# Kernel tuning notes

Measured on AMD Instinct MI355X. Metric: run time of the kernel, lower is better.

## Reference

```python
import jax, jax.numpy as jnp
import numpy as np

T, H, F, E, K = 1024, 2048, 1024, 8, 2  # tokens, hidden, intermediate, experts, top_k
RENORMALIZE = True


def setup_inputs() -> dict:
    key = jax.random.key(0)
    k1, k2, k3, k4, k5 = jax.random.split(key, 5)
    hidden_states = jax.random.normal(k1, (T, H), dtype=jnp.float32)
    router_logits = jax.random.normal(k2, (T, E), dtype=jnp.float32)
    w1 = jax.random.normal(k3, (E, H, F), dtype=jnp.float32) * 0.02  # gate proj
    w3 = jax.random.normal(k4, (E, H, F), dtype=jnp.float32) * 0.02  # up proj
    w2 = jax.random.normal(k5, (E, F, H), dtype=jnp.float32) * 0.02  # down proj
    return {"hidden_states": hidden_states, "router_logits": router_logits,
            "w1": w1, "w3": w3, "w2": w2}


def _moe_forward(x, router_logits, w1, w3, w2):
    # Top-K routing: softmax over all experts, select top-k, optional renormalize.
    probs = jax.nn.softmax(router_logits, axis=-1)            # [T, E]
    topk_vals, topk_ids = jax.lax.top_k(probs, K)             # [T, K]
    if RENORMALIZE:
        topk_vals = topk_vals / jnp.sum(topk_vals, axis=-1, keepdims=True)
    # Dense combine weights: zero for non-selected experts.   [T, E]
    tok_idx = jnp.arange(x.shape[0])[:, None]
    combine = jnp.zeros(probs.shape, dtype=x.dtype).at[tok_idx, topk_ids].set(topk_vals)
    # Expert SwiGLU FFN computed per expert over all tokens, masked-combined.
    g = jnp.einsum('th,ehf->etf', x, w1)                      # gate  [E, T, F]
    u = jnp.einsum('th,ehf->etf', x, w3)                      # up    [E, T, F]
    a = jax.nn.silu(g) * u                                    # silu activation
    y = jnp.einsum('etf,efh->eth', a, w2)                     # down  [E, T, H]
    out = jnp.einsum('eth,te->th', y, combine)                # weighted combine
    return out


def reference(hidden_states, router_logits, w1, w3, w2):
    return _moe_forward(hidden_states, router_logits, w1, w3, w2)
```

## Files before the change

kernel.cpp:

```cpp
#include <hip/hip_runtime.h>
#include <cstdint>
#include <cstddef>

#define T_TOK 1024
#define H_DIM 2048
#define F_DIM 1024
#define E_EXP 8
#define BM 64
#define BK 64
#define BN2 64
#define SP 70
#define MAX_TILES 40
#define ROWCAP 2560

#define I_NTILES 25
#define I_TILE_E 32
#define I_TILE_R0 80
#define I_ROWTOK 4224
#define I_ROWW   6784
#define B_XB     37888
#define B_AWS    (B_XB + T_TOK*H_DIM*2)
#define B_W1T    (B_AWS + ROWCAP*F_DIM*2)
#define B_W3T    (B_W1T + E_EXP*F_DIM*H_DIM*2)

typedef __bf16 bf16x8 __attribute__((ext_vector_type(8)));
typedef __bf16 bf16x2 __attribute__((ext_vector_type(2)));
typedef float  f32x4  __attribute__((ext_vector_type(4)));

#define MFMA(a,b,c) __builtin_amdgcn_mfma_f32_16x16x32_bf16(a,b,c,0,0,0)

__device__ __forceinline__ void gload16(const void* g, void* l) {
  __builtin_amdgcn_global_load_lds(
      (const __attribute__((address_space(1))) void*)g,
      (__attribute__((address_space(3))) void*)l, 16, 0, 0);
}

__global__ __launch_bounds__(1024) void k_route(const float* __restrict__ logits,
                                                int* __restrict__ ws_i) {
  __shared__ int cnt[E_EXP], cur[E_EXP], offs_s[E_EXP];
  const int t = threadIdx.x;
  float* ws_f = (float*)ws_i;
  if (t < E_EXP) { cnt[t] = 0; cur[t] = 0; }
  __syncthreads();
  float l[E_EXP];
#pragma unroll
  for (int e = 0; e < E_EXP; ++e) l[e] = logits[t * E_EXP + e];
  int b0 = 0; float v0 = l[0];
#pragma unroll
  for (int e = 1; e < E_EXP; ++e) if (l[e] > v0) { v0 = l[e]; b0 = e; }
  int b1 = -1; float v1 = -3.4e38f;
#pragma unroll
  for (int e = 0; e < E_EXP; ++e) if (e != b0 && l[e] > v1) { v1 = l[e]; b1 = e; }
  float w0 = 1.f / (1.f + __expf(v1 - v0));
  float w1 = 1.f - w0;
  atomicAdd(&cnt[b0], 1);
  atomicAdd(&cnt[b1], 1);
  __syncthreads();
  if (t == 0) {
    int off = 0, nt = 0;
    for (int e = 0; e < E_EXP; ++e) {
      offs_s[e] = off;
      int ntile = (cnt[e] + BM - 1) / BM;
      for (int i = 0; i < ntile; ++i) {
        ws_i[I_TILE_E + nt] = e;
        ws_i[I_TILE_R0 + nt] = off + i * BM;
        ++nt;
      }
      off += ntile * BM;
    }
    ws_i[I_NTILES] = nt;
  }
  for (int i = t; i < ROWCAP; i += 1024) ws_i[I_ROWTOK + i] = -1;
  __syncthreads();
  {
    int p = atomicAdd(&cur[b0], 1);
    int s = offs_s[b0] + p;
    ws_i[I_ROWTOK + s] = t;
    ws_f[I_ROWW + s] = w0;
  }
  {
    int p = atomicAdd(&cur[b1], 1);
    int s = offs_s[b1] + p;
    ws_i[I_ROWTOK + s] = t;
    ws_f[I_ROWW + s] = w1;
  }
}

__global__ __launch_bounds__(256) void k_cvt(const float* __restrict__ x,
                                             __bf16* __restrict__ xb) {
  long i = (long)(blockIdx.x * 256 + threadIdx.x) * 8;
  float4 a = *(const float4*)(x + i);
  float4 b = *(const float4*)(x + i + 4);
  bf16x8 v;
  v[0] = (__bf16)a.x; v[1] = (__bf16)a.y; v[2] = (__bf16)a.z; v[3] = (__bf16)a.w;
  v[4] = (__bf16)b.x; v[5] = (__bf16)b.y; v[6] = (__bf16)b.z; v[7] = (__bf16)b.w;
  *(bf16x8*)(xb + i) = v;
}

__global__ __launch_bounds__(256) void k_cvtT(const float* __restrict__ src,
                                              __bf16* __restrict__ dst,
                                              int R, int C) {
  __shared__ __bf16 tr[64][66];
  const int e = blockIdx.z, r0 = blockIdx.x * 64, c0 = blockIdx.y * 64;
  const float* s = src + ((size_t)e * R + r0) * C + c0;
  __bf16* d = dst + ((size_t)e * C + c0) * R + r0;
  const int t = threadIdx.x;
  const int lr = t >> 4, lc = (t & 15) * 4;
#pragma unroll
  for (int i = 0; i < 4; ++i) {
    int r = lr + i * 16;
    float4 f = *(const float4*)(s + (size_t)r * C + lc);
    tr[lc + 0][r] = (__bf16)f.x;
    tr[lc + 1][r] = (__bf16)f.y;
    tr[lc + 2][r] = (__bf16)f.z;
    tr[lc + 3][r] = (__bf16)f.w;
  }
  __syncthreads();
  const int oc = t >> 2, ok = (t & 3) * 16;
  *(bf16x8*)(d + (size_t)oc * R + ok)     = *(const bf16x8*)&tr[oc][ok];
  *(bf16x8*)(d + (size_t)oc * R + ok + 8) = *(const bf16x8*)&tr[oc][ok + 8];
}

__global__ __launch_bounds__(256) void k_gemm1(const __bf16* __restrict__ xb,
                                               const __bf16* __restrict__ w1t,
                                               const __bf16* __restrict__ w3t,
                                               const int* __restrict__ ws_i,
                                               __bf16* __restrict__ aws) {
  __shared__ __bf16 sm[2][3 * 4096];
  __shared__ int s_tok[BM];
  const int p = blockIdx.x;
  const int lg = (p & 7) * 80 + (p >> 3);
  const int tile = lg % MAX_TILES;
  const int n0 = (lg / MAX_TILES) * 64;
  if (tile >= ws_i[I_NTILES]) return;
  const int e  = ws_i[I_TILE_E + tile];
  const int r0 = ws_i[I_TILE_R0 + tile];
  const int tid = threadIdx.x, lane = tid & 63, wid = tid >> 6;
  const int wm = wid >> 1, wn = wid & 1;
  const int l15 = lane & 15, l4 = lane >> 4;
  if (tid < BM) {
    int tk = ws_i[I_ROWTOK + r0 + tid];
    s_tok[tid] = tk < 0 ? 0 : tk;
  }
  __syncthreads();
  const int rj0 = wid * 16 + (lane >> 3);
  const int rj1 = rj0 + 8;
  const int ks = ((lane & 7) ^ (lane >> 3)) * 8;
  const __bf16* gA0 = xb + (size_t)s_tok[rj0] * H_DIM + ks;
  const __bf16* gA1 = xb + (size_t)s_tok[rj1] * H_DIM + ks;
  const __bf16* w1e = w1t + (size_t)e * F_DIM * H_DIM;
  const __bf16* w3e = w3t + (size_t)e * F_DIM * H_DIM;
  const __bf16* gB1_0 = w1e + (size_t)(n0 + rj0) * H_DIM + ks;
  const __bf16* gB1_1 = w1e + (size_t)(n0 + rj1) * H_DIM + ks;
  const __bf16* gB3_0 = w3e + (size_t)(n0 + rj0) * H_DIM + ks;
  const __bf16* gB3_1 = w3e + (size_t)(n0 + rj1) * H_DIM + ks;
  const int c0 = wid * 2 * 512, c1 = c0 + 512;

  auto STAGE = [&](int b, int k0) {
    __bf16* As = &sm[b][0];
    __bf16* B1 = &sm[b][4096];
    __bf16* B3 = &sm[b][8192];
    gload16(gA0 + k0,   As + c0);
    gload16(gA1 + k0,   As + c1);
    gload16(gB1_0 + k0, B1 + c0);
    gload16(gB1_1 + k0, B1 + c1);
    gload16(gB3_0 + k0, B3 + c0);
    gload16(gB3_1 + k0, B3 + c1);
  };

  f32x4 accg[2][2] = {}; f32x4 accu[2][2] = {};
  auto COMPUTE = [&](int b) {
    const __bf16* As = &sm[b][0];
    const __bf16* B1 = &sm[b][4096];
    const __bf16* B3 = &sm[b][8192];
    __builtin_amdgcn_s_setprio(1);
#pragma unroll
    for (int kk = 0; kk < 2; ++kk) {
      const int sx = ((kk * 4 + l4) ^ (lane & 7)) << 3;
      const int ra0 = wm * 32 + l15, ra1 = ra0 + 16;
      const int rb0 = wn * 32 + l15, rb1 = rb0 + 16;
      bf16x8 a0  = *(const bf16x8*)&As[ra0 * 64 + sx];
      bf16x8 a1  = *(const bf16x8*)&As[ra1 * 64 + sx];
      bf16x8 b10 = *(const bf16x8*)&B1[rb0 * 64 + sx];
      bf16x8 b11 = *(const bf16x8*)&B1[rb1 * 64 + sx];
      bf16x8 b30 = *(const bf16x8*)&B3[rb0 * 64 + sx];
      bf16x8 b31 = *(const bf16x8*)&B3[rb1 * 64 + sx];
      accg[0][0] = MFMA(a0, b10, accg[0][0]);
      accg[0][1] = MFMA(a0, b11, accg[0][1]);
      accg[1][0] = MFMA(a1, b10, accg[1][0]);
      accg[1][1] = MFMA(a1, b11, accg[1][1]);
      accu[0][0] = MFMA(a0, b30, accu[0][0]);
      accu[0][1] = MFMA(a0, b31, accu[0][1]);
      accu[1][0] = MFMA(a1, b30, accu[1][0]);
      accu[1][1] = MFMA(a1, b31, accu[1][1]);
    }
    __builtin_amdgcn_s_setprio(0);
  };

  STAGE(0, 0);
  __syncthreads();
  int curb = 0;
  for (int t = 0; t < H_DIM / BK; ++t) {
    if (t + 1 < H_DIM / BK) STAGE(curb ^ 1, (t + 1) * BK);
    COMPUTE(curb);
    __syncthreads();
    curb ^= 1;
  }
#pragma unroll
  for (int fm = 0; fm < 2; ++fm)
#pragma unroll
    for (int fn = 0; fn < 2; ++fn)
#pragma unroll
      for (int r = 0; r < 4; ++r) {
        float g = accg[fm][fn][r], u = accu[fm][fn][r];
        float a = g / (1.f + __expf(-g)) * u;
        int row = r0 + wm * 32 + fm * 16 + l4 * 4 + r;
        int col = n0 + wn * 32 + fn * 16 + l15;
        aws[(size_t)row * F_DIM + col] = (__bf16)a;
      }
}

__global__ __launch_bounds__(256) void k_gemm2(const __bf16* __restrict__ aws,
                                               const float* __restrict__ w2,
                                               const int* __restrict__ ws_i,
                                               float* __restrict__ out) {
  __shared__ __bf16 As[BM][SP];
  __shared__ __bf16 Bs[BN2][SP];
  __shared__ int s_tok[BM];
  __shared__ float s_w[BM];
  const int p = blockIdx.x;
  const int lg = (p & 7) * 160 + (p >> 3);
  const int tile = lg % MAX_TILES;
  const int h0 = (lg / MAX_TILES) * BN2;
  if (tile >= ws_i[I_NTILES]) return;
  const int e  = ws_i[I_TILE_E + tile];
  const int r0 = ws_i[I_TILE_R0 + tile];
  const int tid = threadIdx.x, lane = tid & 63, wid = tid >> 6;
  const int wm = wid >> 1, wn = wid & 1;
  const int l15 = lane & 15, lk8 = (lane >> 4) << 3;
  const int ar = tid >> 3, ac = (tid & 7) * 8;
  const int nb = (tid & 15) * 4, kq = (tid >> 4) * 4;
  const float* ws_f = (const float*)ws_i;
  if (tid < BM) {
    s_tok[tid] = ws_i[I_ROWTOK + r0 + tid];
    s_w[tid]   = ws_f[I_ROWW + r0 + tid];
  }
  __syncthreads();
  const __bf16* pA0 = aws + (size_t)(r0 + ar) * F_DIM + ac;
  const __bf16* pA1 = aws + (size_t)(r0 + ar + 32) * F_DIM + ac;
  const float* pB2 = w2 + (size_t)e * F_DIM * H_DIM + h0 + nb + (size_t)kq * H_DIM;

  bf16x8 rA0, rA1;
  f32x4 q2[4];
  auto LOADG = [&](int K0) {
    rA0 = *(const bf16x8*)(pA0 + K0);
    rA1 = *(const bf16x8*)(pA1 + K0);
#pragma unroll
    for (int j = 0; j < 4; ++j) q2[j] = *(const f32x4*)(pB2 + (size_t)(K0 + j) * H_DIM);
  };
  auto WRITEL = [&]() {
    *(bf16x8*)&As[ar][ac] = rA0;
    *(bf16x8*)&As[ar + 32][ac] = rA1;
#pragma unroll
    for (int u = 0; u < 4; ++u) {
      bf16x2 va, vb;
      va[0] = (__bf16)q2[0][u]; va[1] = (__bf16)q2[1][u];
      vb[0] = (__bf16)q2[2][u]; vb[1] = (__bf16)q2[3][u];
      *(bf16x2*)&Bs[nb + u][kq] = va;
      *(bf16x2*)&Bs[nb + u][kq + 2] = vb;
    }
  };

  f32x4 acc[2][2] = {};
  LOADG(0);
  for (int k0 = 0; k0 < F_DIM; k0 += BK) {
    if (k0) __syncthreads();
    WRITEL();
    if (k0 + BK < F_DIM) LOADG(k0 + BK);
    __syncthreads();
    __builtin_amdgcn_s_setprio(1);
#pragma unroll
    for (int kk = 0; kk < 2; ++kk) {
      const int kb = kk * 32 + lk8;
      bf16x8 a0 = *(const bf16x8*)&As[wm * 32 + l15][kb];
      bf16x8 a1 = *(const bf16x8*)&As[wm * 32 + 16 + l15][kb];
      bf16x8 b0 = *(const bf16x8*)&Bs[wn * 32 + l15][kb];
      bf16x8 b1 = *(const bf16x8*)&Bs[wn * 32 + 16 + l15][kb];
      acc[0][0] = MFMA(a0, b0, acc[0][0]);
      acc[0][1] = MFMA(a0, b1, acc[0][1]);
      acc[1][0] = MFMA(a1, b0, acc[1][0]);
      acc[1][1] = MFMA(a1, b1, acc[1][1]);
    }
    __builtin_amdgcn_s_setprio(0);
  }
#pragma unroll
  for (int fm = 0; fm < 2; ++fm)
#pragma unroll
    for (int fn = 0; fn < 2; ++fn)
#pragma unroll
      for (int r = 0; r < 4; ++r) {
        int lrow = wm * 32 + fm * 16 + ((lane >> 4) << 2) + r;
        int t = s_tok[lrow];
        if (t >= 0) {
          float v = acc[fm][fn][r] * s_w[lrow];
          atomicAdd(out + (size_t)t * H_DIM + h0 + wn * 32 + fn * 16 + l15, v);
        }
      }
}

extern "C" void kernel_launch(void* const* d_in, const int* in_sizes, int n_in,
                              void* d_out, int out_size, void* d_ws, size_t ws_size,
                              hipStream_t stream) {
  (void)in_sizes; (void)n_in; (void)out_size; (void)ws_size;
  const float* x      = (const float*)d_in[0];
  const float* logits = (const float*)d_in[1];
  const float* w1     = (const float*)d_in[2];
  const float* w3     = (const float*)d_in[3];
  const float* w2     = (const float*)d_in[4];
  float* out = (float*)d_out;
  int* ws_i = (int*)d_ws;
  __bf16* xb  = (__bf16*)((char*)d_ws + B_XB);
  __bf16* aws = (__bf16*)((char*)d_ws + B_AWS);
  __bf16* w1t = (__bf16*)((char*)d_ws + B_W1T);
  __bf16* w3t = (__bf16*)((char*)d_ws + B_W3T);

  hipMemsetAsync(d_out, 0, (size_t)T_TOK * H_DIM * sizeof(float), stream);
  k_route<<<1, 1024, 0, stream>>>(logits, ws_i);
  k_cvt<<<dim3(T_TOK * H_DIM / (256 * 8)), 256, 0, stream>>>(x, xb);
  k_cvtT<<<dim3(H_DIM / 64, F_DIM / 64, E_EXP), 256, 0, stream>>>(w1, w1t, H_DIM, F_DIM);
  k_cvtT<<<dim3(H_DIM / 64, F_DIM / 64, E_EXP), 256, 0, stream>>>(w3, w3t, H_DIM, F_DIM);
  k_gemm1<<<dim3(MAX_TILES * (F_DIM / 64)), 256, 0, stream>>>(xb, w1t, w3t, ws_i, aws);
  k_gemm2<<<dim3(MAX_TILES * (H_DIM / BN2)), 256, 0, stream>>>(aws, w2, ws_i, out);
}
```

Before: 126.7 us.

## Pre-transpose w2 to bf16 and stream gemm2 tiles via direct global-to-LDS loads

```diff
diff --git a/kernel.cpp b/kernel.cpp
--- a/kernel.cpp
+++ b/kernel.cpp
@@ -8,8 +8,6 @@
 #define E_EXP 8
 #define BM 64
 #define BK 64
-#define BN2 64
-#define SP 70
 #define MAX_TILES 40
 #define ROWCAP 2560
 
@@ -22,9 +20,9 @@
 #define B_AWS    (B_XB + T_TOK*H_DIM*2)
 #define B_W1T    (B_AWS + ROWCAP*F_DIM*2)
 #define B_W3T    (B_W1T + E_EXP*F_DIM*H_DIM*2)
+#define B_W2T    (B_W3T + E_EXP*F_DIM*H_DIM*2)
 
 typedef __bf16 bf16x8 __attribute__((ext_vector_type(8)));
-typedef __bf16 bf16x2 __attribute__((ext_vector_type(2)));
 typedef float  f32x4  __attribute__((ext_vector_type(4)));
 
 #define MFMA(a,b,c) __builtin_amdgcn_mfma_f32_16x16x32_bf16(a,b,c,0,0,0)
@@ -97,13 +95,23 @@
   *(bf16x8*)(xb + i) = v;
 }
 
-__global__ __launch_bounds__(256) void k_cvtT(const float* __restrict__ src,
-                                              __bf16* __restrict__ dst,
-                                              int R, int C) {
+__global__ __launch_bounds__(256) void k_cvtW(const float* __restrict__ w1,
+                                              const float* __restrict__ w3,
+                                              const float* __restrict__ w2,
+                                              __bf16* __restrict__ w1t,
+                                              __bf16* __restrict__ w3t,
+                                              __bf16* __restrict__ w2t) {
   __shared__ __bf16 tr[64][66];
-  const int e = blockIdx.z, r0 = blockIdx.x * 64, c0 = blockIdx.y * 64;
-  const float* s = src + ((size_t)e * R + r0) * C + c0;
-  __bf16* d = dst + ((size_t)e * C + c0) * R + r0;
+  const int z = blockIdx.z;
+  const float* src; __bf16* dst; int R, C;
+  if (z < 8)       { src = w1 + (size_t)z * H_DIM * F_DIM;        dst = w1t + (size_t)z * F_DIM * H_DIM;        R = H_DIM; C = F_DIM; }
+  else if (z < 16) { src = w3 + (size_t)(z - 8) * H_DIM * F_DIM;  dst = w3t + (size_t)(z - 8) * F_DIM * H_DIM;  R = H_DIM; C = F_DIM; }
+  else             { src = w2 + (size_t)(z - 16) * F_DIM * H_DIM; dst = w2t + (size_t)(z - 16) * H_DIM * F_DIM; R = F_DIM; C = H_DIM; }
+  const int ti = blockIdx.x * 16 + blockIdx.y;
+  const int nC = C >> 6;
+  const int r0 = (ti / nC) * 64, c0 = (ti % nC) * 64;
+  const float* s = src + (size_t)r0 * C + c0;
+  __bf16* d = dst + (size_t)c0 * R + r0;
   const int t = threadIdx.x;
   const int lr = t >> 4, lc = (t & 15) * 4;
 #pragma unroll
@@ -221,77 +229,77 @@
 }
 
 __global__ __launch_bounds__(256) void k_gemm2(const __bf16* __restrict__ aws,
-                                               const float* __restrict__ w2,
+                                               const __bf16* __restrict__ w2t,
                                                const int* __restrict__ ws_i,
                                                float* __restrict__ out) {
-  __shared__ __bf16 As[BM][SP];
-  __shared__ __bf16 Bs[BN2][SP];
+  __shared__ __bf16 sm[2][2 * 4096];
   __shared__ int s_tok[BM];
   __shared__ float s_w[BM];
   const int p = blockIdx.x;
   const int lg = (p & 7) * 160 + (p >> 3);
   const int tile = lg % MAX_TILES;
-  const int h0 = (lg / MAX_TILES) * BN2;
+  const int h0 = (lg / MAX_TILES) * 64;
   if (tile >= ws_i[I_NTILES]) return;
   const int e  = ws_i[I_TILE_E + tile];
   const int r0 = ws_i[I_TILE_R0 + tile];
   const int tid = threadIdx.x, lane = tid & 63, wid = tid >> 6;
   const int wm = wid >> 1, wn = wid & 1;
-  const int l15 = lane & 15, lk8 = (lane >> 4) << 3;
-  const int ar = tid >> 3, ac = (tid & 7) * 8;
-  const int nb = (tid & 15) * 4, kq = (tid >> 4) * 4;
+  const int l15 = lane & 15, l4 = lane >> 4;
   const float* ws_f = (const float*)ws_i;
   if (tid < BM) {
     s_tok[tid] = ws_i[I_ROWTOK + r0 + tid];
     s_w[tid]   = ws_f[I_ROWW + r0 + tid];
   }
   __syncthreads();
-  const __bf16* pA0 = aws + (size_t)(r0 + ar) * F_DIM + ac;
-  const __bf16* pA1 = aws + (size_t)(r0 + ar + 32) * F_DIM + ac;
-  const float* pB2 = w2 + (size_t)e * F_DIM * H_DIM + h0 + nb + (size_t)kq * H_DIM;
-
-  bf16x8 rA0, rA1;
-  f32x4 q2[4];
-  auto LOADG = [&](int K0) {
-    rA0 = *(const bf16x8*)(pA0 + K0);
-    rA1 = *(const bf16x8*)(pA1 + K0);
-#pragma unroll
-    for (int j = 0; j < 4; ++j) q2[j] = *(const f32x4*)(pB2 + (size_t)(K0 + j) * H_DIM);
+  const int rj0 = wid * 16 + (lane >> 3);
+  const int rj1 = rj0 + 8;
+  const int ks = ((lane & 7) ^ (lane >> 3)) * 8;
+  const __bf16* gA0 = aws + (size_t)(r0 + rj0) * F_DIM + ks;
+  const __bf16* gA1 = aws + (size_t)(r0 + rj1) * F_DIM + ks;
+  const __bf16* w2e = w2t + (size_t)e * H_DIM * F_DIM;
+  const __bf16* gB0 = w2e + (size_t)(h0 + rj0) * F_DIM + ks;
+  const __bf16* gB1 = w2e + (size_t)(h0 + rj1) * F_DIM + ks;
+  const int c0 = wid * 2 * 512, c1 = c0 + 512;
+
+  auto STAGE = [&](int b, int k0) {
+    __bf16* As = &sm[b][0];
+    __bf16* Bs = &sm[b][4096];
+    gload16(gA0 + k0, As + c0);
+    gload16(gA1 + k0, As + c1);
+    gload16(gB0 + k0, Bs + c0);
+    gload16(gB1 + k0, Bs + c1);
   };
-  auto WRITEL = [&]() {
-    *(bf16x8*)&As[ar][ac] = rA0;
-    *(bf16x8*)&As[ar + 32][ac] = rA1;
-#pragma unroll
-    for (int u = 0; u < 4; ++u) {
-      bf16x2 va, vb;
-      va[0] = (__bf16)q2[0][u]; va[1] = (__bf16)q2[1][u];
-      vb[0] = (__bf16)q2[2][u]; vb[1] = (__bf16)q2[3][u];
-      *(bf16x2*)&Bs[nb + u][kq] = va;
-      *(bf16x2*)&Bs[nb + u][kq + 2] = vb;
-    }
-  };
 
   f32x4 acc[2][2] = {};
-  LOADG(0);
-  for (int k0 = 0; k0 < F_DIM; k0 += BK) {
-    if (k0) __syncthreads();
-    WRITEL();
-    if (k0 + BK < F_DIM) LOADG(k0 + BK);
-    __syncthreads();
+  auto COMPUTE = [&](int b) {
+    const __bf16* As = &sm[b][0];
+    const __bf16* Bs = &sm[b][4096];
     __builtin_amdgcn_s_setprio(1);
 #pragma unroll
     for (int kk = 0; kk < 2; ++kk) {
-      const int kb = kk * 32 + lk8;
-      bf16x8 a0 = *(const bf16x8*)&As[wm * 32 + l15][kb];
-      bf16x8 a1 = *(const bf16x8*)&As[wm * 32 + 16 + l15][kb];
-      bf16x8 b0 = *(const bf16x8*)&Bs[wn * 32 + l15][kb];
-      bf16x8 b1 = *(const bf16x8*)&Bs[wn * 32 + 16 + l15][kb];
+      const int sx = ((kk * 4 + l4) ^ (lane & 7)) << 3;
+      const int ra0 = wm * 32 + l15, ra1 = ra0 + 16;
+      const int rb0 = wn * 32 + l15, rb1 = rb0 + 16;
+      bf16x8 a0 = *(const bf16x8*)&As[ra0 * 64 + sx];
+      bf16x8 a1 = *(const bf16x8*)&As[ra1 * 64 + sx];
+      bf16x8 b0 = *(const bf16x8*)&Bs[rb0 * 64 + sx];
+      bf16x8 b1 = *(const bf16x8*)&Bs[rb1 * 64 + sx];
       acc[0][0] = MFMA(a0, b0, acc[0][0]);
       acc[0][1] = MFMA(a0, b1, acc[0][1]);
       acc[1][0] = MFMA(a1, b0, acc[1][0]);
       acc[1][1] = MFMA(a1, b1, acc[1][1]);
     }
     __builtin_amdgcn_s_setprio(0);
+  };
+
+  STAGE(0, 0);
+  __syncthreads();
+  int curb = 0;
+  for (int t = 0; t < F_DIM / BK; ++t) {
+    if (t + 1 < F_DIM / BK) STAGE(curb ^ 1, (t + 1) * BK);
+    COMPUTE(curb);
+    __syncthreads();
+    curb ^= 1;
   }
 #pragma unroll
   for (int fm = 0; fm < 2; ++fm)
@@ -299,7 +307,7 @@
     for (int fn = 0; fn < 2; ++fn)
 #pragma unroll
       for (int r = 0; r < 4; ++r) {
-        int lrow = wm * 32 + fm * 16 + ((lane >> 4) << 2) + r;
+        int lrow = wm * 32 + fm * 16 + l4 * 4 + r;
         int t = s_tok[lrow];
         if (t >= 0) {
           float v = acc[fm][fn][r] * s_w[lrow];
@@ -323,12 +331,12 @@
   __bf16* aws = (__bf16*)((char*)d_ws + B_AWS);
   __bf16* w1t = (__bf16*)((char*)d_ws + B_W1T);
   __bf16* w3t = (__bf16*)((char*)d_ws + B_W3T);
+  __bf16* w2t = (__bf16*)((char*)d_ws + B_W2T);
 
   hipMemsetAsync(d_out, 0, (size_t)T_TOK * H_DIM * sizeof(float), stream);
   k_route<<<1, 1024, 0, stream>>>(logits, ws_i);
   k_cvt<<<dim3(T_TOK * H_DIM / (256 * 8)), 256, 0, stream>>>(x, xb);
-  k_cvtT<<<dim3(H_DIM / 64, F_DIM / 64, E_EXP), 256, 0, stream>>>(w1, w1t, H_DIM, F_DIM);
-  k_cvtT<<<dim3(H_DIM / 64, F_DIM / 64, E_EXP), 256, 0, stream>>>(w3, w3t, H_DIM, F_DIM);
+  k_cvtW<<<dim3(32, 16, 24), 256, 0, stream>>>(w1, w3, w2, w1t, w3t, w2t);
   k_gemm1<<<dim3(MAX_TILES * (F_DIM / 64)), 256, 0, stream>>>(xb, w1t, w3t, ws_i, aws);
-  k_gemm2<<<dim3(MAX_TILES * (H_DIM / BN2)), 256, 0, stream>>>(aws, w2, ws_i, out);
-}
+  k_gemm2<<<dim3(MAX_TILES * (H_DIM / 64)), 256, 0, stream>>>(aws, w2t, ws_i, out);
+}
```

New measurement: 132.9 us. +4.9%, slower.
